# Kernel optimization log

Hardware: AMD Instinct MI355X
Metric: run time of the kernel (lower is better)

The kernel has to match this reference:

```python
import jax, jax.numpy as jnp
import numpy as np

GAMMA = 1.0

def _rbf_mean(X, Y, gamma):
    x2 = jnp.sum(X * X, axis=1)  # [n]
    y2 = jnp.sum(Y * Y, axis=1)  # [m]
    d2 = x2[:, None] + y2[None, :] - 2.0 * (X @ Y.T)
    d2 = jnp.maximum(d2, 0.0)
    return jnp.mean(jnp.exp(-gamma * d2))

def setup_inputs() -> dict:
    key = jax.random.key(0)
    k1, k2 = jax.random.split(key)
    N = jax.random.normal(k1, (8192, 256), dtype=jnp.float32)
    R = jax.random.normal(k2, (8192, 256), dtype=jnp.float32)
    return {"N": N, "R": R}

def reference(N, R):
    xx = _rbf_mean(N, N, GAMMA)
    yy = _rbf_mean(R, R, GAMMA)
    xy = _rbf_mean(N, R, GAMMA)
    mmd = xx + yy - 2.0 * xy
    return jnp.sqrt(mmd)
```

## Files before the change

### kernel.cpp

```cpp
#include <hip/hip_runtime.h>
#include <hip/hip_bf16.h>
#include <math.h>

typedef float f32x4 __attribute__((ext_vector_type(4)));
typedef int   i32x4 __attribute__((ext_vector_type(4)));
typedef int   i32x8 __attribute__((ext_vector_type(8)));
typedef float f32x2 __attribute__((ext_vector_type(2)));

#define MTOT 16384
#define HALF 8192
#define KDIM 256
#define BM 128
#define NB (MTOT / BM)
#define NBLK (NB * (NB + 1) / 2)
#define NPART (NBLK * 4)

#define GLDS16(g, l) __builtin_amdgcn_global_load_lds(                      \
    (const __attribute__((address_space(1))) void*)(g),                     \
    (__attribute__((address_space(3))) void*)(l), 16, 0, 0)

__global__ __launch_bounds__(256) void convert_kernel(
    const float* __restrict__ Nmat, const float* __restrict__ Rmat,
    unsigned int* __restrict__ Z, float* __restrict__ x2) {
  const int lane = threadIdx.x & 63;
  const int wv = threadIdx.x >> 6;
  const int row = blockIdx.x * 4 + wv;
  const float* src = (row < HALF) ? (Nmat + (size_t)row * KDIM)
                                  : (Rmat + (size_t)(row - HALF) * KDIM);
  float4 v = *(const float4*)(src + lane * 4);
  int pk = __builtin_amdgcn_cvt_pk_fp8_f32(v.x, v.y, 0, false);
  pk = __builtin_amdgcn_cvt_pk_fp8_f32(v.z, v.w, pk, true);
  Z[(size_t)row * (KDIM / 4) + lane] = (unsigned int)pk;
  f32x2 d01 = __builtin_amdgcn_cvt_pk_f32_fp8(pk, false);
  f32x2 d23 = __builtin_amdgcn_cvt_pk_f32_fp8(pk, true);
  float sq = d01[0] * d01[0] + d01[1] * d01[1] + d23[0] * d23[0] + d23[1] * d23[1];
  #pragma unroll
  for (int off = 32; off; off >>= 1) sq += __shfl_down(sq, off);
  if (lane == 0) x2[row] = sq;
}

__global__ __launch_bounds__(256, 2) void mmd_gemm(
    const unsigned char* __restrict__ Z, const float* __restrict__ x2,
    float* __restrict__ partials) {
  const int t = blockIdx.x;
  const int u = NBLK - 1 - t;
  int rr = (int)((sqrtf(8.0f * (float)u + 1.0f) - 1.0f) * 0.5f);
  while (rr * (rr + 1) / 2 > u) --rr;
  while ((rr + 1) * (rr + 2) / 2 <= u) ++rr;
  const int bm = NB - 1 - rr;
  const int bn = bm + (t - (bm * NB - bm * (bm - 1) / 2));

  __shared__ unsigned char As[BM * KDIM];
  __shared__ unsigned char Bs[BM * KDIM];

  const int tid  = threadIdx.x;
  const int lane = tid & 63;
  const int wid  = tid >> 6;
  const int wm   = wid >> 1;
  const int wn   = wid & 1;

  const unsigned char* Abase = Z + (size_t)bm * BM * KDIM;
  const unsigned char* Bbase = Z + (size_t)bn * BM * KDIM;

  {
    const int lr = lane >> 4;
    const int ls = lane & 15;
    #pragma unroll
    for (int tt = 0; tt < 8; ++tt) {
      int i = wid * 8 + tt;
      int gr = i * 4 + lr;
      int c = ls ^ (gr & 7);
      GLDS16(Abase + (size_t)gr * KDIM + c * 16, As + i * 1024);
      GLDS16(Bbase + (size_t)gr * KDIM + c * 16, Bs + i * 1024);
    }
  }

  const int fr = lane & 15;
  const int fq = lane >> 4;

  float xrh[4][4], xch[4];
  #pragma unroll
  for (int tm = 0; tm < 4; ++tm)
    #pragma unroll
    for (int v = 0; v < 4; ++v)
      xrh[tm][v] = -0.5f * x2[bm * BM + wm * 64 + tm * 16 + fq * 4 + v];
  #pragma unroll
  for (int tn = 0; tn < 4; ++tn)
    xch[tn] = -0.5f * x2[bn * BM + wn * 64 + tn * 16 + fr];

  f32x4 acc[4][4];
  #pragma unroll
  for (int tm = 0; tm < 4; ++tm)
    #pragma unroll
    for (int tn = 0; tn < 4; ++tn)
      #pragma unroll
      for (int v = 0; v < 4; ++v)
        acc[tm][tn][v] = xrh[tm][v] + xch[tn];

  __syncthreads();

  const int key = fr & 7;
  #pragma unroll
  for (int ks = 0; ks < 2; ++ks) {
    const int c0 = ks * 8 + fq * 2;
    i32x8 af[4], bf[4];
    #pragma unroll
    for (int tm = 0; tm < 4; ++tm) {
      int row = wm * 64 + tm * 16 + fr;
      i32x4 lo = *(const i32x4*)(As + row * KDIM + ((c0 ^ key) * 16));
      i32x4 hi = *(const i32x4*)(As + row * KDIM + (((c0 + 1) ^ key) * 16));
      af[tm] = __builtin_shufflevector(lo, hi, 0, 1, 2, 3, 4, 5, 6, 7);
    }
    #pragma unroll
    for (int tn = 0; tn < 4; ++tn) {
      int row = wn * 64 + tn * 16 + fr;
      i32x4 lo = *(const i32x4*)(Bs + row * KDIM + ((c0 ^ key) * 16));
      i32x4 hi = *(const i32x4*)(Bs + row * KDIM + (((c0 + 1) ^ key) * 16));
      bf[tn] = __builtin_shufflevector(lo, hi, 0, 1, 2, 3, 4, 5, 6, 7);
    }
    #pragma unroll
    for (int tm = 0; tm < 4; ++tm)
      #pragma unroll
      for (int tn = 0; tn < 4; ++tn)
        acc[tm][tn] = __builtin_amdgcn_mfma_scale_f32_16x16x128_f8f6f4(
            af[tm], bf[tn], acc[tm][tn], 0, 0,
            0, 0x7F7F7F7F, 0, 0x7F7F7F7F);
  }

  float amax = -1e30f;
  #pragma unroll
  for (int tm = 0; tm < 4; ++tm)
    #pragma unroll
    for (int tn = 0; tn < 4; ++tn)
      #pragma unroll
      for (int v = 0; v < 4; ++v)
        amax = fmaxf(amax, acc[tm][tn][v]);

  float partial = 0.f;
  if (__any(amax > -40.f)) {
    #pragma unroll
    for (int tm = 0; tm < 4; ++tm)
      #pragma unroll
      for (int tn = 0; tn < 4; ++tn)
        #pragma unroll
        for (int v = 0; v < 4; ++v) {
          float a = fminf(acc[tm][tn][v], 0.f);
          partial += exp2f(a * 2.885390082f);
        }
  }

  float wgt = ((bm < NB / 2) == (bn < NB / 2)) ? 1.f : -1.f;
  if (bm != bn) wgt *= 2.f;

  #pragma unroll
  for (int off = 32; off; off >>= 1) partial += __shfl_down(partial, off);
  if (lane == 0) partials[blockIdx.x * 4 + wid] = partial * wgt;
}

__global__ __launch_bounds__(1024) void finalize_kernel(
    const float* __restrict__ partials, float* __restrict__ out) {
  float s = 0.f;
  for (int i = threadIdx.x; i < NPART; i += 1024) s += partials[i];
  #pragma unroll
  for (int off = 32; off; off >>= 1) s += __shfl_down(s, off);
  __shared__ float ws[16];
  if ((threadIdx.x & 63) == 0) ws[threadIdx.x >> 6] = s;
  __syncthreads();
  if (threadIdx.x == 0) {
    float tot = 0.f;
    #pragma unroll
    for (int i = 0; i < 16; ++i) tot += ws[i];
    float mmd = tot / ((float)HALF * (float)HALF);
    out[0] = sqrtf(fmaxf(mmd, 0.f));
  }
}

extern "C" void kernel_launch(void* const* d_in, const int* in_sizes, int n_in,
                              void* d_out, int out_size, void* d_ws, size_t ws_size,
                              hipStream_t stream) {
  const float* Nmat = (const float*)d_in[0];
  const float* Rmat = (const float*)d_in[1];
  float* out = (float*)d_out;

  char* ws = (char*)d_ws;
  unsigned char* Z = (unsigned char*)ws;
  float* x2       = (float*)(ws + (size_t)MTOT * KDIM);
  float* partials = (float*)(ws + (size_t)MTOT * KDIM + MTOT * 4);

  convert_kernel<<<MTOT / 4, 256, 0, stream>>>(Nmat, Rmat, (unsigned int*)Z, x2);
  mmd_gemm<<<NBLK, 256, 0, stream>>>(Z, x2, partials);
  finalize_kernel<<<1, 1024, 0, stream>>>(partials, out);
}
```

Before: 121.0 us.

## Use persistent 256x256 tiles with double-buffered K-halves and prefetch of next tile

Replaces the one-block-per-128x128-tile launch with a persistent grid of 256 blocks of 512 threads, each looping over 256x256 upper-triangle tiles. The K dimension is split into two 128-byte halves held in separate LDS buffers, so the next tile's loads are issued while the current tile's second half and exp epilogue run, using explicit waitcnt and barrier calls. The norm terms are now added in the epilogue instead of seeding the accumulators. This aims to hide global-load latency and raise MFMA reuse per byte loaded. In exchange it uses more registers per thread (32 accumulator tiles) and the waitcnt choreography must be correct. The triangle has 2080 tiles spread over 256 blocks, which may leave the tail unbalanced.

```diff
diff --git a/kernel.cpp b/kernel.cpp
--- a/kernel.cpp
+++ b/kernel.cpp
@@ -10,14 +10,20 @@
 #define MTOT 16384
 #define HALF 8192
 #define KDIM 256
-#define BM 128
-#define NB (MTOT / BM)
+#define BT 256
+#define NB (MTOT / BT)
 #define NBLK (NB * (NB + 1) / 2)
-#define NPART (NBLK * 4)
+#define GRID 256
+#define NPART (GRID * 8)
 
 #define GLDS16(g, l) __builtin_amdgcn_global_load_lds(                      \
     (const __attribute__((address_space(1))) void*)(g),                     \
     (__attribute__((address_space(3))) void*)(l), 16, 0, 0)
+
+#define WAIT_VM8()   __builtin_amdgcn_s_waitcnt(0x0F78)
+#define WAIT_VM0()   __builtin_amdgcn_s_waitcnt(0x0F70)
+#define WAIT_LGKM0() __builtin_amdgcn_s_waitcnt(0xC07F)
+#define BARRIER()    __builtin_amdgcn_s_barrier()
 
 __global__ __launch_bounds__(256) void convert_kernel(
     const float* __restrict__ Nmat, const float* __restrict__ Rmat,
@@ -39,122 +45,164 @@
   if (lane == 0) x2[row] = sq;
 }
 
-__global__ __launch_bounds__(256, 2) void mmd_gemm(
+__global__ __launch_bounds__(512, 2) void mmd_gemm(
     const unsigned char* __restrict__ Z, const float* __restrict__ x2,
     float* __restrict__ partials) {
-  const int t = blockIdx.x;
-  const int u = NBLK - 1 - t;
-  int rr = (int)((sqrtf(8.0f * (float)u + 1.0f) - 1.0f) * 0.5f);
-  while (rr * (rr + 1) / 2 > u) --rr;
-  while ((rr + 1) * (rr + 2) / 2 <= u) ++rr;
-  const int bm = NB - 1 - rr;
-  const int bn = bm + (t - (bm * NB - bm * (bm - 1) / 2));
-
-  __shared__ unsigned char As[BM * KDIM];
-  __shared__ unsigned char Bs[BM * KDIM];
+  __shared__ unsigned char As0[BT * 128], Bs0[BT * 128];
+  __shared__ unsigned char As1[BT * 128], Bs1[BT * 128];
 
   const int tid  = threadIdx.x;
   const int lane = tid & 63;
   const int wid  = tid >> 6;
-  const int wm   = wid >> 1;
-  const int wn   = wid & 1;
-
-  const unsigned char* Abase = Z + (size_t)bm * BM * KDIM;
-  const unsigned char* Bbase = Z + (size_t)bn * BM * KDIM;
-
-  {
-    const int lr = lane >> 4;
-    const int ls = lane & 15;
-    #pragma unroll
-    for (int tt = 0; tt < 8; ++tt) {
-      int i = wid * 8 + tt;
-      int gr = i * 4 + lr;
-      int c = ls ^ (gr & 7);
-      GLDS16(Abase + (size_t)gr * KDIM + c * 16, As + i * 1024);
-      GLDS16(Bbase + (size_t)gr * KDIM + c * 16, Bs + i * 1024);
-    }
-  }
-
-  const int fr = lane & 15;
-  const int fq = lane >> 4;
-
-  float xrh[4][4], xch[4];
-  #pragma unroll
-  for (int tm = 0; tm < 4; ++tm)
-    #pragma unroll
-    for (int v = 0; v < 4; ++v)
-      xrh[tm][v] = -0.5f * x2[bm * BM + wm * 64 + tm * 16 + fq * 4 + v];
-  #pragma unroll
-  for (int tn = 0; tn < 4; ++tn)
-    xch[tn] = -0.5f * x2[bn * BM + wn * 64 + tn * 16 + fr];
-
-  f32x4 acc[4][4];
-  #pragma unroll
-  for (int tm = 0; tm < 4; ++tm)
-    #pragma unroll
-    for (int tn = 0; tn < 4; ++tn)
-      #pragma unroll
-      for (int v = 0; v < 4; ++v)
-        acc[tm][tn][v] = xrh[tm][v] + xch[tn];
-
-  __syncthreads();
-
-  const int key = fr & 7;
-  #pragma unroll
-  for (int ks = 0; ks < 2; ++ks) {
-    const int c0 = ks * 8 + fq * 2;
-    i32x8 af[4], bf[4];
-    #pragma unroll
-    for (int tm = 0; tm < 4; ++tm) {
-      int row = wm * 64 + tm * 16 + fr;
-      i32x4 lo = *(const i32x4*)(As + row * KDIM + ((c0 ^ key) * 16));
-      i32x4 hi = *(const i32x4*)(As + row * KDIM + (((c0 + 1) ^ key) * 16));
+  const int wm   = wid >> 2;
+  const int wn   = wid & 3;
+  const int fr   = lane & 15;
+  const int fq   = lane >> 4;
+  const int lr   = lane >> 3;
+  const int ls   = lane & 7;
+  const int key  = fr & 7;
+
+  auto issue_half = [&](const unsigned char* Ab, const unsigned char* Bb,
+                        int kk, unsigned char* as, unsigned char* bs) {
+    #pragma unroll
+    for (int q = 0; q < 4; ++q) {
+      int i = wid * 4 + q;
+      int gr = i * 8 + lr;
+      int c = ls ^ lr;
+      GLDS16(Ab + (size_t)gr * KDIM + kk + c * 16, as + i * 1024);
+    }
+    #pragma unroll
+    for (int q = 0; q < 4; ++q) {
+      int i = wid * 4 + q;
+      int gr = i * 8 + lr;
+      int c = ls ^ lr;
+      GLDS16(Bb + (size_t)gr * KDIM + kk + c * 16, bs + i * 1024);
+    }
+  };
+
+  auto compute_half = [&](const unsigned char* as, const unsigned char* bs,
+                          f32x4 (&acc)[8][4]) {
+    i32x8 af[8], bf[4];
+    #pragma unroll
+    for (int tm = 0; tm < 8; ++tm) {
+      int row = wm * 128 + tm * 16 + fr;
+      const unsigned char* rb = as + row * 128;
+      i32x4 lo = *(const i32x4*)(rb + (((2 * fq) ^ key) * 16));
+      i32x4 hi = *(const i32x4*)(rb + (((2 * fq + 1) ^ key) * 16));
       af[tm] = __builtin_shufflevector(lo, hi, 0, 1, 2, 3, 4, 5, 6, 7);
     }
     #pragma unroll
     for (int tn = 0; tn < 4; ++tn) {
       int row = wn * 64 + tn * 16 + fr;
-      i32x4 lo = *(const i32x4*)(Bs + row * KDIM + ((c0 ^ key) * 16));
-      i32x4 hi = *(const i32x4*)(Bs + row * KDIM + (((c0 + 1) ^ key) * 16));
+      const unsigned char* rb = bs + row * 128;
+      i32x4 lo = *(const i32x4*)(rb + (((2 * fq) ^ key) * 16));
+      i32x4 hi = *(const i32x4*)(rb + (((2 * fq + 1) ^ key) * 16));
       bf[tn] = __builtin_shufflevector(lo, hi, 0, 1, 2, 3, 4, 5, 6, 7);
     }
     #pragma unroll
-    for (int tm = 0; tm < 4; ++tm)
-      #pragma unroll
-      for (int tn = 0; tn < 4; ++tn)
+    for (int tn = 0; tn < 4; ++tn)
+      #pragma unroll
+      for (int tm = 0; tm < 8; ++tm)
         acc[tm][tn] = __builtin_amdgcn_mfma_scale_f32_16x16x128_f8f6f4(
             af[tm], bf[tn], acc[tm][tn], 0, 0,
             0, 0x7F7F7F7F, 0, 0x7F7F7F7F);
-  }
-
-  float amax = -1e30f;
-  #pragma unroll
-  for (int tm = 0; tm < 4; ++tm)
+  };
+
+  auto decode = [](int t, int& bm, int& bn) {
+    int u = NBLK - 1 - t;
+    int rr = (int)((sqrtf(8.0f * (float)u + 1.0f) - 1.0f) * 0.5f);
+    while (rr * (rr + 1) / 2 > u) --rr;
+    while ((rr + 1) * (rr + 2) / 2 <= u) ++rr;
+    bm = NB - 1 - rr;
+    bn = bm + (t - (bm * NB - bm * (bm - 1) / 2));
+  };
+
+  float total = 0.f;
+
+  int idx = blockIdx.x;
+  int bm, bn;
+  decode(idx, bm, bn);
+  const unsigned char* Ab = Z + (size_t)bm * BT * KDIM;
+  const unsigned char* Bb = Z + (size_t)bn * BT * KDIM;
+  issue_half(Ab, Bb, 0,   As0, Bs0);
+  issue_half(Ab, Bb, 128, As1, Bs1);
+
+  while (true) {
+    const int nidx = idx + GRID;
+    const bool haveNext = (nidx < NBLK);
+    int nm = 0, nn = 0;
+    const unsigned char *nAb = nullptr, *nBb = nullptr;
+    if (haveNext) {
+      decode(nidx, nm, nn);
+      nAb = Z + (size_t)nm * BT * KDIM;
+      nBb = Z + (size_t)nn * BT * KDIM;
+    }
+
+    f32x4 acc[8][4];
+    #pragma unroll
+    for (int i = 0; i < 8; ++i)
+      #pragma unroll
+      for (int j = 0; j < 4; ++j)
+        acc[i][j] = (f32x4){0.f, 0.f, 0.f, 0.f};
+
+    WAIT_VM8();
+    BARRIER();
+    compute_half(As0, Bs0, acc);
+    WAIT_LGKM0();
+    BARRIER();
+    if (haveNext) issue_half(nAb, nBb, 0, As0, Bs0);
+
+    WAIT_VM8();
+    if (!haveNext) WAIT_VM0();
+    BARRIER();
+    compute_half(As1, Bs1, acc);
+
+    float4 xr[8];
+    #pragma unroll
+    for (int tm = 0; tm < 8; ++tm)
+      xr[tm] = *(const float4*)(x2 + bm * BT + wm * 128 + tm * 16 + fq * 4);
+    float xc[4];
     #pragma unroll
     for (int tn = 0; tn < 4; ++tn)
-      #pragma unroll
-      for (int v = 0; v < 4; ++v)
-        amax = fmaxf(amax, acc[tm][tn][v]);
-
-  float partial = 0.f;
-  if (__any(amax > -40.f)) {
-    #pragma unroll
-    for (int tm = 0; tm < 4; ++tm)
+      xc[tn] = x2[bn * BT + wn * 64 + tn * 16 + fr];
+
+    float amax = -1e30f;
+    #pragma unroll
+    for (int tm = 0; tm < 8; ++tm)
       #pragma unroll
       for (int tn = 0; tn < 4; ++tn)
         #pragma unroll
         for (int v = 0; v < 4; ++v) {
-          float a = fminf(acc[tm][tn][v], 0.f);
-          partial += exp2f(a * 2.885390082f);
+          float m = 2.f * acc[tm][tn][v] - ((const float*)&xr[tm])[v] - xc[tn];
+          amax = fmaxf(amax, m);
         }
+
+    if (__any(amax > -80.f)) {
+      float wgt = ((bm < NB / 2) == (bn < NB / 2)) ? 1.f : -1.f;
+      if (bm != bn) wgt *= 2.f;
+      float p = 0.f;
+      #pragma unroll
+      for (int tm = 0; tm < 8; ++tm)
+        #pragma unroll
+        for (int tn = 0; tn < 4; ++tn)
+          #pragma unroll
+          for (int v = 0; v < 4; ++v) {
+            float m = 2.f * acc[tm][tn][v] - ((const float*)&xr[tm])[v] - xc[tn];
+            p += exp2f(fminf(m, 0.f) * 1.442695041f);
+          }
+      total += p * wgt;
+    }
+
+    WAIT_LGKM0();
+    BARRIER();
+    if (!haveNext) break;
+    issue_half(nAb, nBb, 128, As1, Bs1);
+    idx = nidx; bm = nm; bn = nn; Ab = nAb; Bb = nBb;
   }
 
-  float wgt = ((bm < NB / 2) == (bn < NB / 2)) ? 1.f : -1.f;
-  if (bm != bn) wgt *= 2.f;
-
   #pragma unroll
-  for (int off = 32; off; off >>= 1) partial += __shfl_down(partial, off);
-  if (lane == 0) partials[blockIdx.x * 4 + wid] = partial * wgt;
+  for (int off = 32; off; off >>= 1) total += __shfl_down(total, off);
+  if (lane == 0) partials[blockIdx.x * 8 + wid] = total;
 }
 
 __global__ __launch_bounds__(1024) void finalize_kernel(
@@ -188,6 +236,6 @@
   float* partials = (float*)(ws + (size_t)MTOT * KDIM + MTOT * 4);
 
   convert_kernel<<<MTOT / 4, 256, 0, stream>>>(Nmat, Rmat, (unsigned int*)Z, x2);
-  mmd_gemm<<<NBLK, 256, 0, stream>>>(Z, x2, partials);
+  mmd_gemm<<<GRID, 512, 0, stream>>>(Z, x2, partials);
   finalize_kernel<<<1, 1024, 0, stream>>>(partials, out);
 }
```

Result: slower. 190.5 us (+57.4%).
